# Kernel optimization log

Hardware: AMD Instinct MI355X
Metric: run time of the kernel (lower is better)

## Reference

```python
import jax, jax.numpy as jnp
import numpy as np

EMBED_DIM = 1024
NUM_HEADS = 16
HEAD_DIM = EMBED_DIM // NUM_HEADS
HIDDEN_DIM = int(EMBED_DIM * 4.0)
LN_EPS = 1e-5


def layer_norm(x, g, b):
    mu = jnp.mean(x, axis=-1, keepdims=True)
    var = jnp.var(x, axis=-1, keepdims=True)
    return (x - mu) * jax.lax.rsqrt(var + LN_EPS) * g + b


def setup_inputs() -> dict:
    key = jax.random.key(0)
    ks = jax.random.split(key, 8)
    D, H3, Dh = EMBED_DIM, 3 * EMBED_DIM, HIDDEN_DIM
    s = lambda fan: 1.0 / np.sqrt(fan)
    return {
        "x": jax.random.normal(ks[0], (2, 2048, D), dtype=jnp.float32),
        "ln1_g": jnp.ones((D,), jnp.float32),
        "ln1_b": jnp.zeros((D,), jnp.float32),
        "ln2_g": jnp.ones((D,), jnp.float32),
        "ln2_b": jnp.zeros((D,), jnp.float32),
        "w_qkv": jax.random.normal(ks[1], (D, H3), jnp.float32) * s(D),
        "b_qkv": jnp.zeros((H3,), jnp.float32),
        "w_proj": jax.random.normal(ks[2], (D, D), jnp.float32) * s(D),
        "b_proj": jnp.zeros((D,), jnp.float32),
        "w_fc1": jax.random.normal(ks[3], (D, Dh), jnp.float32) * s(D),
        "b_fc1": jnp.zeros((Dh,), jnp.float32),
        "w_fc2": jax.random.normal(ks[4], (Dh, D), jnp.float32) * s(Dh),
        "b_fc2": jnp.zeros((D,), jnp.float32),
    }


def reference(x, ln1_g, ln1_b, ln2_g, ln2_b, w_qkv, b_qkv, w_proj, b_proj,
              w_fc1, b_fc1, w_fc2, b_fc2):
    B, N, D = x.shape
    H, hd = NUM_HEADS, HEAD_DIM

    # --- attention branch (dropout inactive at eval) ---
    h = layer_norm(x, ln1_g, ln1_b)
    qkv = h @ w_qkv + b_qkv                      # [B,N,3D]
    qkv = qkv.reshape(B, N, 3, H, hd)
    q = qkv[:, :, 0].transpose(0, 2, 1, 3)       # [B,H,N,hd]
    k = qkv[:, :, 1].transpose(0, 2, 1, 3)
    v = qkv[:, :, 2].transpose(0, 2, 1, 3)
    scores = jnp.einsum('bhqd,bhkd->bhqk', q, k) / jnp.sqrt(jnp.float32(hd))
    attn = jax.nn.softmax(scores, axis=-1)
    ctx = jnp.einsum('bhqk,bhkd->bhqd', attn, v) # [B,H,N,hd]
    ctx = ctx.transpose(0, 2, 1, 3).reshape(B, N, D)
    x = x + ctx @ w_proj + b_proj

    # --- MLP branch ---
    h2 = layer_norm(x, ln2_g, ln2_b)
    h2 = jax.nn.gelu(h2 @ w_fc1 + b_fc1, approximate=False)  # torch nn.GELU = exact erf
    x = x + h2 @ w_fc2 + b_fc2
    return x
```

## Files before the change

kernel.cpp:

```cpp
#include <hip/hip_runtime.h>
#include <hip/hip_bf16.h>
#include <cstdint>

typedef __attribute__((ext_vector_type(8))) short short8;
typedef __attribute__((ext_vector_type(4))) float f32x4;

__device__ __forceinline__ uint16_t f2b(float f) {
  uint32_t u = __builtin_bit_cast(uint32_t, f);
  return (uint16_t)((u + 0x7FFFu + ((u >> 16) & 1u)) >> 16);
}
__device__ __forceinline__ float b2f(uint16_t h) {
  uint32_t u = ((uint32_t)h) << 16;
  return __builtin_bit_cast(float, u);
}
__device__ __forceinline__ void async16(void* lds, const void* g) {
  __builtin_amdgcn_global_load_lds(
      (const __attribute__((address_space(1))) uint32_t*)g,
      (__attribute__((address_space(3))) uint32_t*)lds, 16, 0, 0);
}
__device__ __forceinline__ void xcd_remap(int& bx, int& by, int& bz) {
  int gx = gridDim.x, gy = gridDim.y;
  int nwg = gx * gy * gridDim.z;
  int hw = blockIdx.x + gx * (blockIdx.y + gy * blockIdx.z);
  int work = ((nwg & 7) == 0) ? ((hw & 7) * (nwg >> 3) + (hw >> 3)) : hw;
  bx = work % gx;
  int t = work / gx;
  by = t % gy;
  bz = t / gy;
}

__global__ __launch_bounds__(256) void k_transpose_all(
    const float* __restrict__ wq, const float* __restrict__ wp,
    const float* __restrict__ w1, const float* __restrict__ w2,
    uint16_t* __restrict__ tq, uint16_t* __restrict__ tp,
    uint16_t* __restrict__ t1, uint16_t* __restrict__ t2) {
  __shared__ float tile[64][65];
  int id = blockIdx.x;
  const float* w; uint16_t* wT; int K, N, bx, by;
  if (id < 768)        { w = wq; wT = tq; K = 1024; N = 3072; bx = id % 48; by = id / 48; }
  else if (id < 1024)  { id -= 768;  w = wp; wT = tp; K = 1024; N = 1024; bx = id & 15; by = id >> 4; }
  else if (id < 2048)  { id -= 1024; w = w1; wT = t1; K = 1024; N = 4096; bx = id & 63; by = id >> 6; }
  else                 { id -= 2048; w = w2; wT = t2; K = 4096; N = 1024; bx = id & 15; by = id >> 4; }
  const int tx = threadIdx.x;
  const int k0 = by * 64, n0 = bx * 64;
  const int cr = tx & 15, rbase = tx >> 4;
#pragma unroll
  for (int rr = 0; rr < 4; ++rr) {
    int k = rbase + rr * 16;
    int n = cr * 4;
    float4 v = *(const float4*)&w[(size_t)(k0 + k) * N + (n0 + n)];
    tile[k][n + 0] = v.x; tile[k][n + 1] = v.y;
    tile[k][n + 2] = v.z; tile[k][n + 3] = v.w;
  }
  __syncthreads();
#pragma unroll
  for (int rr = 0; rr < 4; ++rr) {
    int n = rbase + rr * 16;
    int k = cr * 4;
    ushort4 o;
    o.x = f2b(tile[k + 0][n]);
    o.y = f2b(tile[k + 1][n]);
    o.z = f2b(tile[k + 2][n]);
    o.w = f2b(tile[k + 3][n]);
    *(ushort4*)&wT[(size_t)(n0 + n) * K + (k0 + k)] = o;
  }
}

__global__ __launch_bounds__(256) void k_layernorm(
    const float* __restrict__ x, const float* __restrict__ g,
    const float* __restrict__ b, uint16_t* __restrict__ out) {
  const int row = blockIdx.x * 4 + (threadIdx.x >> 6);
  const int lane = threadIdx.x & 63;
  const float* xr = x + (size_t)row * 1024;
  float4 v[4];
  float s = 0.f, ss = 0.f;
#pragma unroll
  for (int i = 0; i < 4; ++i) {
    v[i] = *(const float4*)&xr[i * 256 + lane * 4];
    s += v[i].x + v[i].y + v[i].z + v[i].w;
    ss += v[i].x * v[i].x + v[i].y * v[i].y + v[i].z * v[i].z + v[i].w * v[i].w;
  }
#pragma unroll
  for (int off = 1; off < 64; off <<= 1) {
    s += __shfl_xor(s, off);
    ss += __shfl_xor(ss, off);
  }
  float mu = s * (1.f / 1024.f);
  float rstd = rsqrtf(ss * (1.f / 1024.f) - mu * mu + 1e-5f);
#pragma unroll
  for (int i = 0; i < 4; ++i) {
    int col = i * 256 + lane * 4;
    float4 gv = *(const float4*)&g[col];
    float4 bv = *(const float4*)&b[col];
    ushort4 o;
    o.x = f2b((v[i].x - mu) * rstd * gv.x + bv.x);
    o.y = f2b((v[i].y - mu) * rstd * gv.y + bv.y);
    o.z = f2b((v[i].z - mu) * rstd * gv.z + bv.z);
    o.w = f2b((v[i].w - mu) * rstd * gv.w + bv.w);
    *(ushort4*)&out[(size_t)row * 1024 + col] = o;
  }
}

__global__ __launch_bounds__(256) void k_ln2_fuse(
    const float* __restrict__ x, const uint16_t* __restrict__ pp0,
    const uint16_t* __restrict__ pp1, const float* __restrict__ bias,
    const float* __restrict__ g, const float* __restrict__ b,
    float* __restrict__ x2, uint16_t* __restrict__ out) {
  const int row = blockIdx.x * 4 + (threadIdx.x >> 6);
  const int lane = threadIdx.x & 63;
  const size_t rb = (size_t)row * 1024;
  float4 v[4];
  float s = 0.f, ss = 0.f;
#pragma unroll
  for (int i = 0; i < 4; ++i) {
    int col = i * 256 + lane * 4;
    float4 xv = *(const float4*)&x[rb + col];
    float4 bv = *(const float4*)&bias[col];
    ushort4 a0 = *(const ushort4*)&pp0[rb + col];
    ushort4 a1 = *(const ushort4*)&pp1[rb + col];
    v[i].x = xv.x + bv.x + b2f(a0.x) + b2f(a1.x);
    v[i].y = xv.y + bv.y + b2f(a0.y) + b2f(a1.y);
    v[i].z = xv.z + bv.z + b2f(a0.z) + b2f(a1.z);
    v[i].w = xv.w + bv.w + b2f(a0.w) + b2f(a1.w);
    *(float4*)&x2[rb + col] = v[i];
    s += v[i].x + v[i].y + v[i].z + v[i].w;
    ss += v[i].x * v[i].x + v[i].y * v[i].y + v[i].z * v[i].z + v[i].w * v[i].w;
  }
#pragma unroll
  for (int off = 1; off < 64; off <<= 1) {
    s += __shfl_xor(s, off);
    ss += __shfl_xor(ss, off);
  }
  float mu = s * (1.f / 1024.f);
  float rstd = rsqrtf(ss * (1.f / 1024.f) - mu * mu + 1e-5f);
#pragma unroll
  for (int i = 0; i < 4; ++i) {
    int col = i * 256 + lane * 4;
    float4 gv = *(const float4*)&g[col];
    float4 bv = *(const float4*)&b[col];
    ushort4 o;
    o.x = f2b((v[i].x - mu) * rstd * gv.x + bv.x);
    o.y = f2b((v[i].y - mu) * rstd * gv.y + bv.y);
    o.z = f2b((v[i].z - mu) * rstd * gv.z + bv.z);
    o.w = f2b((v[i].w - mu) * rstd * gv.w + bv.w);
    *(ushort4*)&out[rb + col] = o;
  }
}

__global__ __launch_bounds__(256) void k_fc2_reduce(
    const float* __restrict__ x2, const uint16_t* __restrict__ f0,
    const uint16_t* __restrict__ f1, const float* __restrict__ bias,
    float* __restrict__ out, int N) {
  int i = (blockIdx.x * 256 + threadIdx.x) * 4;
  float4 v = *(const float4*)&x2[i];
  float4 bv = *(const float4*)&bias[i & (N - 1)];
  ushort4 a0 = *(const ushort4*)&f0[i];
  ushort4 a1 = *(const ushort4*)&f1[i];
  v.x += bv.x + b2f(a0.x) + b2f(a1.x);
  v.y += bv.y + b2f(a0.y) + b2f(a1.y);
  v.z += bv.z + b2f(a0.z) + b2f(a1.z);
  v.w += bv.w + b2f(a0.w) + b2f(a1.w);
  *(float4*)&out[i] = v;
}

template <int EPI>
__global__ __launch_bounds__(256) void k_gemm(
    const uint16_t* __restrict__ A, const uint16_t* __restrict__ Bt,
    const float* __restrict__ bias, void* __restrict__ Cout,
    uint16_t* __restrict__ vTout, int M, int N, int K) {
  __shared__ __align__(16) uint16_t Alds[128 * 64];
  __shared__ __align__(16) uint16_t Blds[128 * 64];
  int bx, by, bz;
  xcd_remap(bx, by, bz);
  const int tid = threadIdx.x;
  const int lane = tid & 63;
  const int w = tid >> 6;
  const int wr = w >> 1, wc = w & 1;
  const int m0 = by * 128, n0 = bx * 128;
  const int l15 = lane & 15, l4 = lane >> 4;
  const uint16_t* pA[4];
  const uint16_t* pB[4];
#pragma unroll
  for (int c = 0; c < 4; ++c) {
    int i = c * 256 + tid;
    int row = i >> 3, d = (i & 7) * 8;
    pA[c] = A + (size_t)(m0 + row) * K + d;
    pB[c] = Bt + (size_t)(n0 + row) * K + d;
  }
  f32x4 acc[4][4] = {};
  for (int k0 = 0; k0 < K; k0 += 64) {
#pragma unroll
    for (int c = 0; c < 4; ++c) {
      async16(&Alds[(c * 256 + tid) * 8], pA[c]);
      pA[c] += 64;
    }
#pragma unroll
    for (int c = 0; c < 4; ++c) {
      async16(&Blds[(c * 256 + tid) * 8], pB[c]);
      pB[c] += 64;
    }
    __syncthreads();
#pragma unroll
    for (int kc = 0; kc < 2; ++kc) {
      short8 af[4], bf[4];
#pragma unroll
      for (int m = 0; m < 4; ++m)
        af[m] = *(const short8*)&Alds[(wr * 64 + m * 16 + l15) * 64 + kc * 32 + l4 * 8];
#pragma unroll
      for (int n = 0; n < 4; ++n)
        bf[n] = *(const short8*)&Blds[(wc * 64 + n * 16 + l15) * 64 + kc * 32 + l4 * 8];
#pragma unroll
      for (int m = 0; m < 4; ++m)
#pragma unroll
        for (int n = 0; n < 4; ++n)
          acc[m][n] = __builtin_amdgcn_mfma_f32_16x16x32_bf16(af[m], bf[n], acc[m][n], 0, 0, 0);
    }
    __syncthreads();
  }
#pragma unroll
  for (int m = 0; m < 4; ++m) {
#pragma unroll
    for (int n = 0; n < 4; ++n) {
      int col = n0 + wc * 64 + n * 16 + l15;
      int rowb = m0 + wr * 64 + m * 16 + l4 * 4;
      float bv = bias[col];
      if constexpr (EPI == 3) {
        if (col >= 2048) {
          int dtot = col - 2048;
          int hh = dtot >> 6, dd = dtot & 63;
          int bg = rowb >> 11, tl = rowb & 2047;
          ushort4 ov;
          ov.x = f2b(acc[m][n][0] + bv);
          ov.y = f2b(acc[m][n][1] + bv);
          ov.z = f2b(acc[m][n][2] + bv);
          ov.w = f2b(acc[m][n][3] + bv);
          *(ushort4*)&vTout[(((size_t)(bg * 16 + hh)) * 64 + dd) * 2048 + tl] = ov;
          continue;
        }
      }
#pragma unroll
      for (int r = 0; r < 4; ++r) {
        float val = acc[m][n][r] + bv;
        size_t idx = (size_t)(rowb + r) * N + col;
        if constexpr (EPI == 2) {
          float u = val * val;
          float a = fmaf(u, 0.1029480545f, 2.3022078158f);
          float t = exp2f(val * a);
          float gl = val - val / (t + 1.0f);
          ((uint16_t*)Cout)[idx] = f2b(gl);
        } else {
          ((uint16_t*)Cout)[idx] = f2b(val);
        }
      }
    }
  }
}

__global__ __launch_bounds__(256) void k_gemm_splitk(
    const uint16_t* __restrict__ A, const uint16_t* __restrict__ Bt,
    uint16_t* __restrict__ p0, uint16_t* __restrict__ p1,
    int M, int N, int K, int Kc) {
  __shared__ __align__(16) uint16_t Alds[128 * 64];
  __shared__ __align__(16) uint16_t Blds[128 * 64];
  int bx, by, bz;
  xcd_remap(bx, by, bz);
  const int tid = threadIdx.x;
  const int lane = tid & 63;
  const int w = tid >> 6;
  const int wr = w >> 1, wc = w & 1;
  const int m0 = by * 128, n0 = bx * 128;
  const int l15 = lane & 15, l4 = lane >> 4;
  const int kbeg = bz * Kc;
  uint16_t* __restrict__ P = (bz == 0) ? p0 : p1;
  const uint16_t* pA[4];
  const uint16_t* pB[4];
#pragma unroll
  for (int c = 0; c < 4; ++c) {
    int i = c * 256 + tid;
    int row = i >> 3, d = (i & 7) * 8;
    pA[c] = A + (size_t)(m0 + row) * K + kbeg + d;
    pB[c] = Bt + (size_t)(n0 + row) * K + kbeg + d;
  }
  f32x4 acc[4][4] = {};
  for (int k0 = 0; k0 < Kc; k0 += 64) {
#pragma unroll
    for (int c = 0; c < 4; ++c) {
      async16(&Alds[(c * 256 + tid) * 8], pA[c]);
      pA[c] += 64;
    }
#pragma unroll
    for (int c = 0; c < 4; ++c) {
      async16(&Blds[(c * 256 + tid) * 8], pB[c]);
      pB[c] += 64;
    }
    __syncthreads();
#pragma unroll
    for (int kc = 0; kc < 2; ++kc) {
      short8 af[4], bf[4];
#pragma unroll
      for (int m = 0; m < 4; ++m)
        af[m] = *(const short8*)&Alds[(wr * 64 + m * 16 + l15) * 64 + kc * 32 + l4 * 8];
#pragma unroll
      for (int n = 0; n < 4; ++n)
        bf[n] = *(const short8*)&Blds[(wc * 64 + n * 16 + l15) * 64 + kc * 32 + l4 * 8];
#pragma unroll
      for (int m = 0; m < 4; ++m)
#pragma unroll
        for (int n = 0; n < 4; ++n)
          acc[m][n] = __builtin_amdgcn_mfma_f32_16x16x32_bf16(af[m], bf[n], acc[m][n], 0, 0, 0);
    }
    __syncthreads();
  }
#pragma unroll
  for (int m = 0; m < 4; ++m) {
#pragma unroll
    for (int n = 0; n < 4; ++n) {
      int col = n0 + wc * 64 + n * 16 + l15;
      int rowb = m0 + wr * 64 + m * 16 + l4 * 4;
#pragma unroll
      for (int r = 0; r < 4; ++r)
        P[(size_t)(rowb + r) * N + col] = f2b(acc[m][n][r]);
    }
  }
}

__global__ __launch_bounds__(256, 4) void k_attn(
    const uint16_t* __restrict__ qkv, const uint16_t* __restrict__ vT,
    uint16_t* __restrict__ ctx) {
  __shared__ __align__(16) uint16_t Klds[2][64 * 64];
  __shared__ __align__(16) uint16_t Vlds[2][64 * 64];
  __shared__ __align__(16) uint16_t Plds[4][16 * 64];
  int bx, by, bz;
  xcd_remap(bx, by, bz);
  const int bh = by, qt = bx;
  const int b = bh >> 4, h = bh & 15;
  const int tid = threadIdx.x, lane = tid & 63, w = tid >> 6;
  const int l15 = lane & 15, l4 = lane >> 4;
  const int sw = (l15 & 7) << 3;
  const size_t tokbase = (size_t)b * 2048;

  const float QSC = 0.125f * 1.44269504088896340736f;
  short8 qa[2];
  const int qrow = qt * 64 + w * 16 + l15;
#pragma unroll
  for (int kc = 0; kc < 2; ++kc) {
    short8 v = *(const short8*)&qkv[(tokbase + qrow) * 3072 + h * 64 + kc * 32 + l4 * 8];
#pragma unroll
    for (int j = 0; j < 8; ++j) v[j] = (short)f2b(b2f((uint16_t)v[j]) * QSC);
    qa[kc] = v;
  }
  short8 ones;
#pragma unroll
  for (int j = 0; j < 8; ++j) ones[j] = (short)0x3F80;

  float m_s = -1e30f;
  f32x4 o[4] = {};
  f32x4 ol = {};

  const uint16_t* pK[2];
  const uint16_t* pV[2];
#pragma unroll
  for (int c = 0; c < 2; ++c) {
    int i = c * 256 + tid;
    int row = i >> 3, colE = (i & 7) * 8;
    int colS = colE ^ ((row & 7) << 3);
    pK[c] = qkv + (tokbase + row) * 3072 + 1024 + h * 64 + colS;
    pV[c] = vT + ((size_t)bh * 64 + row) * 2048 + colS;
  }

  auto stage = [&](int buf) {
#pragma unroll
    for (int c = 0; c < 2; ++c) {
      async16(&Klds[buf][(c * 256 + tid) * 8], pK[c]);
      pK[c] += 64 * 3072;
    }
#pragma unroll
    for (int c = 0; c < 2; ++c) {
      async16(&Vlds[buf][(c * 256 + tid) * 8], pV[c]);
      pV[c] += 64;
    }
  };

  stage(0);
  __syncthreads();
  int cur = 0;

  for (int t0 = 0; t0 < 2048; t0 += 64) {
    if (t0 + 64 < 2048) stage(cur ^ 1);

    f32x4 s[4] = {};
    __builtin_amdgcn_s_setprio(1);
#pragma unroll
    for (int kc = 0; kc < 2; ++kc) {
      const int cc = (kc * 32 + l4 * 8) ^ sw;
#pragma unroll
      for (int c = 0; c < 4; ++c) {
        short8 kf = *(const short8*)&Klds[cur][(c * 16 + l15) * 64 + cc];
        s[c] = __builtin_amdgcn_mfma_f32_16x16x32_bf16(kf, qa[kc], s[c], 0, 0, 0);
      }
    }
    __builtin_amdgcn_s_setprio(0);

    {
      float a0 = fmaxf(fmaxf(s[0][0], s[0][1]), fmaxf(s[0][2], s[0][3]));
      float a1 = fmaxf(fmaxf(s[1][0], s[1][1]), fmaxf(s[1][2], s[1][3]));
      float a2 = fmaxf(fmaxf(s[2][0], s[2][1]), fmaxf(s[2][2], s[2][3]));
      float a3 = fmaxf(fmaxf(s[3][0], s[3][1]), fmaxf(s[3][2], s[3][3]));
      float pml = fmaxf(fmaxf(a0, a1), fmaxf(a2, a3));
      if (!__all(pml - m_s <= 8.f)) {
        float pm = pml;
        pm = fmaxf(pm, __shfl_xor(pm, 16));
        pm = fmaxf(pm, __shfl_xor(pm, 32));
        float mn = fmaxf(m_s, pm);
        float scale = exp2f(m_s - mn);
        m_s = mn;
        float sc0 = __shfl(scale, l4 * 4 + 0);
        float sc1 = __shfl(scale, l4 * 4 + 1);
        float sc2 = __shfl(scale, l4 * 4 + 2);
        float sc3 = __shfl(scale, l4 * 4 + 3);
#pragma unroll
        for (int df = 0; df < 4; ++df) {
          o[df][0] *= sc0; o[df][1] *= sc1; o[df][2] *= sc2; o[df][3] *= sc3;
        }
        ol[0] *= sc0; ol[1] *= sc1; ol[2] *= sc2; ol[3] *= sc3;
      }
#pragma unroll
      for (int c = 0; c < 4; ++c) {
        float p0 = exp2f(s[c][0] - m_s);
        float p1 = exp2f(s[c][1] - m_s);
        float p2 = exp2f(s[c][2] - m_s);
        float p3 = exp2f(s[c][3] - m_s);
        uint32_t lo, hi;
        asm("v_cvt_pk_bf16_f32 %0, %1, %2" : "=v"(lo) : "v"(p0), "v"(p1));
        asm("v_cvt_pk_bf16_f32 %0, %1, %2" : "=v"(hi) : "v"(p2), "v"(p3));
        *(uint2*)&Plds[w][l15 * 64 + ((c * 16 + l4 * 4) ^ sw)] = make_uint2(lo, hi);
      }
    }

    __builtin_amdgcn_s_setprio(1);
#pragma unroll
    for (int kc = 0; kc < 2; ++kc) {
      const int cc = (kc * 32 + l4 * 8) ^ sw;
      short8 pa = *(const short8*)&Plds[w][l15 * 64 + cc];
      ol = __builtin_amdgcn_mfma_f32_16x16x32_bf16(pa, ones, ol, 0, 0, 0);
#pragma unroll
      for (int df = 0; df < 4; ++df) {
        short8 vf = *(const short8*)&Vlds[cur][(df * 16 + l15) * 64 + cc];
        o[df] = __builtin_amdgcn_mfma_f32_16x16x32_bf16(pa, vf, o[df], 0, 0, 0);
      }
    }
    __builtin_amdgcn_s_setprio(0);
    __syncthreads();
    cur ^= 1;
  }

#pragma unroll
  for (int r = 0; r < 4; ++r) {
    float rl = 1.0f / ol[r];
    int tok = qt * 64 + w * 16 + l4 * 4 + r;
#pragma unroll
    for (int df = 0; df < 4; ++df) {
      ctx[(tokbase + tok) * 1024 + h * 64 + df * 16 + l15] = f2b(o[df][r] * rl);
    }
  }
}

extern "C" void kernel_launch(void* const* d_in, const int* in_sizes, int n_in,
                              void* d_out, int out_size, void* d_ws, size_t ws_size,
                              hipStream_t stream) {
  const float* x      = (const float*)d_in[0];
  const float* ln1_g  = (const float*)d_in[1];
  const float* ln1_b  = (const float*)d_in[2];
  const float* ln2_g  = (const float*)d_in[3];
  const float* ln2_b  = (const float*)d_in[4];
  const float* w_qkv  = (const float*)d_in[5];
  const float* b_qkv  = (const float*)d_in[6];
  const float* w_proj = (const float*)d_in[7];
  const float* b_proj = (const float*)d_in[8];
  const float* w_fc1  = (const float*)d_in[9];
  const float* b_fc1  = (const float*)d_in[10];
  const float* w_fc2  = (const float*)d_in[11];
  const float* b_fc2  = (const float*)d_in[12];
  float* out = (float*)d_out;
  char* ws = (char*)d_ws;
  const size_t MB = 1 << 20;

  uint16_t* wTfc1  = (uint16_t*)(ws + 0 * MB);
  uint16_t* wTfc2  = (uint16_t*)(ws + 8 * MB);
  uint16_t* wTqkv  = (uint16_t*)(ws + 16 * MB);
  uint16_t* wTproj = (uint16_t*)(ws + 22 * MB);
  uint16_t* hbuf   = (uint16_t*)(ws + 24 * MB);
  uint16_t* qkvb   = (uint16_t*)(ws + 32 * MB);
  uint16_t* vTb    = (uint16_t*)(ws + 56 * MB);
  uint16_t* ctxb   = (uint16_t*)(ws + 64 * MB);
  float*    x2b    = (float*)   (ws + 72 * MB);
  uint16_t* pp0    = (uint16_t*)(ws + 32 * MB);
  uint16_t* pp1    = (uint16_t*)(ws + 40 * MB);
  uint16_t* actb   = (uint16_t*)(ws + 32 * MB);
  uint16_t* fp0    = (uint16_t*)(ws + 16 * MB);
  uint16_t* fp1    = (uint16_t*)(ws + 24 * MB);

  k_transpose_all<<<3072, 256, 0, stream>>>(w_qkv, w_proj, w_fc1, w_fc2,
                                            wTqkv, wTproj, wTfc1, wTfc2);

  k_layernorm<<<1024, 256, 0, stream>>>(x, ln1_g, ln1_b, hbuf);
  k_gemm<3><<<dim3(24, 32), 256, 0, stream>>>(hbuf, wTqkv, b_qkv, qkvb, vTb, 4096, 3072, 1024);
  k_attn<<<dim3(32, 32), 256, 0, stream>>>(qkvb, vTb, ctxb);

  k_gemm_splitk<<<dim3(8, 32, 2), 256, 0, stream>>>(ctxb, wTproj, pp0, pp1,
                                                    4096, 1024, 1024, 512);
  k_ln2_fuse<<<1024, 256, 0, stream>>>(x, pp0, pp1, b_proj, ln2_g, ln2_b, x2b, hbuf);

  k_gemm<2><<<dim3(32, 32), 256, 0, stream>>>(hbuf, wTfc1, b_fc1, actb, nullptr, 4096, 4096, 1024);

  k_gemm_splitk<<<dim3(8, 32, 2), 256, 0, stream>>>(actb, wTfc2, fp0, fp1,
                                                    4096, 1024, 4096, 2048);
  k_fc2_reduce<<<4096, 256, 0, stream>>>(x2b, fp0, fp1, b_fc2, out, 1024);
}
```

Before: 293.2 us.

## Split attention key tiles across two wave groups with intra-block softmax merge

The attention kernel now runs with 512 threads: each query tile is processed by two groups of four waves, each handling half of every 64-key tile (32 keys). Each group keeps its own running max, sum and output accumulators, and at the end group 1 writes its partials to LDS so group 0 can rescale and merge them before the final write. This doubles the wave-level parallelism per block, which is meant to hide latency better and shorten each wave's serial loop. The cost is the final LDS merge step, duplicated Q loads and exp work per group, and changed launch bounds that may limit registers.

```diff
diff --git a/kernel.cpp b/kernel.cpp
--- a/kernel.cpp
+++ b/kernel.cpp
@@ -324,24 +324,26 @@
   }
 }
 
-__global__ __launch_bounds__(256, 4) void k_attn(
+__global__ __launch_bounds__(512, 8) void k_attn(
     const uint16_t* __restrict__ qkv, const uint16_t* __restrict__ vT,
     uint16_t* __restrict__ ctx) {
   __shared__ __align__(16) uint16_t Klds[2][64 * 64];
   __shared__ __align__(16) uint16_t Vlds[2][64 * 64];
-  __shared__ __align__(16) uint16_t Plds[4][16 * 64];
+  __shared__ __align__(16) uint16_t Plds[8][16 * 32];
   int bx, by, bz;
   xcd_remap(bx, by, bz);
   const int bh = by, qt = bx;
   const int b = bh >> 4, h = bh & 15;
-  const int tid = threadIdx.x, lane = tid & 63, w = tid >> 6;
+  const int tid = threadIdx.x, lane = tid & 63, wv = tid >> 6;
+  const int wq = wv & 3;
+  const int g = wv >> 2;
   const int l15 = lane & 15, l4 = lane >> 4;
   const int sw = (l15 & 7) << 3;
   const size_t tokbase = (size_t)b * 2048;
 
   const float QSC = 0.125f * 1.44269504088896340736f;
   short8 qa[2];
-  const int qrow = qt * 64 + w * 16 + l15;
+  const int qrow = qt * 64 + wq * 16 + l15;
 #pragma unroll
   for (int kc = 0; kc < 2; ++kc) {
     short8 v = *(const short8*)&qkv[(tokbase + qrow) * 3072 + h * 64 + kc * 32 + l4 * 8];
@@ -357,28 +359,16 @@
   f32x4 o[4] = {};
   f32x4 ol = {};
 
-  const uint16_t* pK[2];
-  const uint16_t* pV[2];
-#pragma unroll
-  for (int c = 0; c < 2; ++c) {
-    int i = c * 256 + tid;
-    int row = i >> 3, colE = (i & 7) * 8;
-    int colS = colE ^ ((row & 7) << 3);
-    pK[c] = qkv + (tokbase + row) * 3072 + 1024 + h * 64 + colS;
-    pV[c] = vT + ((size_t)bh * 64 + row) * 2048 + colS;
-  }
+  const int srow = tid >> 3;
+  const int scolS = ((tid & 7) * 8) ^ ((srow & 7) << 3);
+  const uint16_t* pK = qkv + (tokbase + srow) * 3072 + 1024 + h * 64 + scolS;
+  const uint16_t* pV = vT + ((size_t)bh * 64 + srow) * 2048 + scolS;
 
   auto stage = [&](int buf) {
-#pragma unroll
-    for (int c = 0; c < 2; ++c) {
-      async16(&Klds[buf][(c * 256 + tid) * 8], pK[c]);
-      pK[c] += 64 * 3072;
-    }
-#pragma unroll
-    for (int c = 0; c < 2; ++c) {
-      async16(&Vlds[buf][(c * 256 + tid) * 8], pV[c]);
-      pV[c] += 64;
-    }
+    async16(&Klds[buf][tid * 8], pK);
+    pK += 64 * 3072;
+    async16(&Vlds[buf][tid * 8], pV);
+    pV += 64;
   };
 
   stage(0);
@@ -388,14 +378,14 @@
   for (int t0 = 0; t0 < 2048; t0 += 64) {
     if (t0 + 64 < 2048) stage(cur ^ 1);
 
-    f32x4 s[4] = {};
+    f32x4 s[2] = {};
     __builtin_amdgcn_s_setprio(1);
 #pragma unroll
     for (int kc = 0; kc < 2; ++kc) {
       const int cc = (kc * 32 + l4 * 8) ^ sw;
 #pragma unroll
-      for (int c = 0; c < 4; ++c) {
-        short8 kf = *(const short8*)&Klds[cur][(c * 16 + l15) * 64 + cc];
+      for (int c = 0; c < 2; ++c) {
+        short8 kf = *(const short8*)&Klds[cur][(g * 32 + c * 16 + l15) * 64 + cc];
         s[c] = __builtin_amdgcn_mfma_f32_16x16x32_bf16(kf, qa[kc], s[c], 0, 0, 0);
       }
     }
@@ -404,9 +394,7 @@
     {
       float a0 = fmaxf(fmaxf(s[0][0], s[0][1]), fmaxf(s[0][2], s[0][3]));
       float a1 = fmaxf(fmaxf(s[1][0], s[1][1]), fmaxf(s[1][2], s[1][3]));
-      float a2 = fmaxf(fmaxf(s[2][0], s[2][1]), fmaxf(s[2][2], s[2][3]));
-      float a3 = fmaxf(fmaxf(s[3][0], s[3][1]), fmaxf(s[3][2], s[3][3]));
-      float pml = fmaxf(fmaxf(a0, a1), fmaxf(a2, a3));
+      float pml = fmaxf(a0, a1);
       if (!__all(pml - m_s <= 8.f)) {
         float pm = pml;
         pm = fmaxf(pm, __shfl_xor(pm, 16));
@@ -425,7 +413,7 @@
         ol[0] *= sc0; ol[1] *= sc1; ol[2] *= sc2; ol[3] *= sc3;
       }
 #pragma unroll
-      for (int c = 0; c < 4; ++c) {
+      for (int c = 0; c < 2; ++c) {
         float p0 = exp2f(s[c][0] - m_s);
         float p1 = exp2f(s[c][1] - m_s);
         float p2 = exp2f(s[c][2] - m_s);
@@ -433,16 +421,15 @@
         uint32_t lo, hi;
         asm("v_cvt_pk_bf16_f32 %0, %1, %2" : "=v"(lo) : "v"(p0), "v"(p1));
         asm("v_cvt_pk_bf16_f32 %0, %1, %2" : "=v"(hi) : "v"(p2), "v"(p3));
-        *(uint2*)&Plds[w][l15 * 64 + ((c * 16 + l4 * 4) ^ sw)] = make_uint2(lo, hi);
+        *(uint2*)&Plds[wv][l15 * 32 + c * 16 + l4 * 4] = make_uint2(lo, hi);
       }
     }
 
     __builtin_amdgcn_s_setprio(1);
-#pragma unroll
-    for (int kc = 0; kc < 2; ++kc) {
-      const int cc = (kc * 32 + l4 * 8) ^ sw;
-      short8 pa = *(const short8*)&Plds[w][l15 * 64 + cc];
+    {
+      short8 pa = *(const short8*)&Plds[wv][l15 * 32 + l4 * 8];
       ol = __builtin_amdgcn_mfma_f32_16x16x32_bf16(pa, ones, ol, 0, 0, 0);
+      const int cc = (g * 32 + l4 * 8) ^ sw;
 #pragma unroll
       for (int df = 0; df < 4; ++df) {
         short8 vf = *(const short8*)&Vlds[cur][(df * 16 + l15) * 64 + cc];
@@ -454,13 +441,42 @@
     cur ^= 1;
   }
 
-#pragma unroll
-  for (int r = 0; r < 4; ++r) {
-    float rl = 1.0f / ol[r];
-    int tok = qt * 64 + w * 16 + l4 * 4 + r;
-#pragma unroll
-    for (int df = 0; df < 4; ++df) {
-      ctx[(tokbase + tok) * 1024 + h * 64 + df * 16 + l15] = f2b(o[df][r] * rl);
+  float* oB  = (float*)&Klds[0][0];
+  float* olB = (float*)&Vlds[0][0];
+  float* mB  = olB + 1024;
+  if (g == 1) {
+#pragma unroll
+    for (int df = 0; df < 4; ++df)
+#pragma unroll
+      for (int r = 0; r < 4; ++r)
+        oB[(df * 4 + r) * 256 + wq * 64 + lane] = o[df][r];
+#pragma unroll
+    for (int r = 0; r < 4; ++r)
+      olB[r * 256 + wq * 64 + lane] = ol[r];
+    mB[wq * 64 + lane] = m_s;
+  }
+  __syncthreads();
+  if (g == 0) {
+    float mBq = mB[wq * 64 + lane];
+    float mq = fmaxf(m_s, mBq);
+    float sAq = exp2f(m_s - mq);
+    float sBq = exp2f(mBq - mq);
+    float sA[4], sB[4];
+#pragma unroll
+    for (int r = 0; r < 4; ++r) {
+      sA[r] = __shfl(sAq, l4 * 4 + r);
+      sB[r] = __shfl(sBq, l4 * 4 + r);
+    }
+#pragma unroll
+    for (int r = 0; r < 4; ++r) {
+      float lT = ol[r] * sA[r] + olB[r * 256 + wq * 64 + lane] * sB[r];
+      float rl = 1.0f / lT;
+      int tok = qt * 64 + wq * 16 + l4 * 4 + r;
+#pragma unroll
+      for (int df = 0; df < 4; ++df) {
+        float val = o[df][r] * sA[r] + oB[(df * 4 + r) * 256 + wq * 64 + lane] * sB[r];
+        ctx[(tokbase + tok) * 1024 + h * 64 + df * 16 + l15] = f2b(val * rl);
+      }
     }
   }
 }
@@ -505,7 +521,7 @@
 
   k_layernorm<<<1024, 256, 0, stream>>>(x, ln1_g, ln1_b, hbuf);
   k_gemm<3><<<dim3(24, 32), 256, 0, stream>>>(hbuf, wTqkv, b_qkv, qkvb, vTb, 4096, 3072, 1024);
-  k_attn<<<dim3(32, 32), 256, 0, stream>>>(qkvb, vTb, ctxb);
+  k_attn<<<dim3(32, 32), 512, 0, stream>>>(qkvb, vTb, ctxb);
 
   k_gemm_splitk<<<dim3(8, 32, 2), 256, 0, stream>>>(ctxb, wTproj, pp0, pp1,
                                                     4096, 1024, 1024, 512);
```

Measured after the change: 303.8 us. 3.6% more time.
